# Kernel tuning notes

Hardware: AMD Instinct MI355X
Metric: run time of the kernel (lower is better)

## Reference

```python
import jax, jax.numpy as jnp
import numpy as np

B, L_PREM, T_HYP, D = 32, 256, 128, 256


def setup_inputs() -> dict:
    key = jax.random.key(0)
    ks = jax.random.split(key, 6)
    scale = 1.0 / np.sqrt(D)
    return {
        "x": jax.random.normal(ks[0], (B, L_PREM + T_HYP, D), dtype=jnp.float32),
        "w_y": jax.random.normal(ks[1], (D, D), dtype=jnp.float32) * scale,
        "w_h": jax.random.normal(ks[2], (D, D), dtype=jnp.float32) * scale,
        "w_r": jax.random.normal(ks[3], (D, D), dtype=jnp.float32) * scale,
        "w_alpha": jax.random.normal(ks[4], (D, 1), dtype=jnp.float32) * scale,
        "w_t": jax.random.normal(ks[5], (D, D), dtype=jnp.float32) * scale,
        "L": L_PREM,
    }


def reference(x, w_y, w_h, w_r, w_alpha, w_t, L):
    # x: (B, L + T, D)
    premise = x[:, :L, :]                 # Y: (B, L, D)
    hypothesis = jnp.swapaxes(x[:, L:, :], 0, 1)  # (T, B, D)

    # Y @ W_y does not depend on t: hoist out of the scan (same math).
    WY = jnp.einsum("bld,de->ble", premise, w_y)  # (B, L, D)

    def step(r_tm1, h_t):
        # r_tm1: (B, D), h_t: (B, D)
        s = h_t @ w_h + r_tm1 @ w_r                 # (B, D)
        Mt = jnp.tanh(WY + s[:, None, :])           # (B, L, D)
        scores = jnp.squeeze(Mt @ w_alpha, -1)      # (B, L)
        alpha = jax.nn.softmax(scores, axis=-1)     # (B, L)
        r_t = jnp.einsum("bl,bld->bd", alpha, premise) + r_tm1 @ w_t
        return r_t, r_t

    r0 = jnp.zeros_like(premise[:, 0, :])           # (B, D)
    _, rs = jax.lax.scan(step, r0, hypothesis)      # rs: (T, B, D)
    return jnp.swapaxes(rs, 0, 1)                   # (B, T, D)
```

## Files before the change

### kernel.cpp

```cpp
#include <hip/hip_runtime.h>
#include <hip/hip_fp16.h>

typedef unsigned long long u64;

#define C2X 2.8853900817779268f
#define LOG2E 1.4426950408889634f

#define WYS_OFF   0u
#define PR_OFF    4194304u
#define PREMH_OFF 8388608u
#define HWH_OFF   12582912u
#define WTH_OFF   16777216u
#define WTR_OFF   16908288u
#define ZP_OFF    17039360u
#define RCH_OFF   18087936u
#define MEMSET_SZ 1179648u

#define PRC_OFF    0u
#define WTRC_OFF   16384u
#define PREMC_OFF  32768u
#define WTC_OFF    49152u
#define WYC_OFF    65536u
#define HWHC_OFF   81920u
#define SCH_OFF    98304u
#define WACH_OFF   98432u
#define RED_OFF    98560u
#define ALB_OFF    98624u
#define RBB_OFF    100672u
#define PART_OFF   101696u
#define LDS_TOTAL  105920u

__global__ __launch_bounds__(256) void prep_all(const float* __restrict__ x,
                                                const float* __restrict__ wy,
                                                const float* __restrict__ wh,
                                                const float* __restrict__ wr,
                                                const float* __restrict__ wt,
                                                __half* __restrict__ wys,
                                                __half* __restrict__ prh,
                                                float* __restrict__ hwh,
                                                __half* __restrict__ wtrh,
                                                __half* __restrict__ premh,
                                                __half* __restrict__ wth) {
    const int blk = blockIdx.x;
    if (blk >= 1568) {
        int i = (blk - 1568) * 256 + threadIdx.x;
        float4 v; __half* dst; int e;
        if (i < 524288) {
            e = i * 4; int b = e >> 16;
            v = *(const float4*)(x + (size_t)e + (size_t)b * 32768);
            dst = premh + e;
        } else if (i < 540672) {
            e = (i - 524288) * 4;
            v = *(const float4*)(wt + e);
            dst = wth + e;
        } else return;
        __half h[4] = {__float2half(v.x),__float2half(v.y),__float2half(v.z),__float2half(v.w)};
        *(uint2*)dst = *(const uint2*)h;
        return;
    }
    __shared__ float At[8][256];
    const int d = threadIdx.x;
    int mode, row0;
    if (blk < 1024)      { mode = 0; row0 = blk * 8; }
    else if (blk < 1536) { mode = 1; row0 = (blk - 1024) * 8; }
    else                 { mode = 2; row0 = (blk - 1536) * 8; }
    for (int rr = 0; rr < 8; ++rr) {
        int r = row0 + rr;
        const float* src;
        if (mode == 0)      { int b = r >> 8, l = r & 255; src = x + (size_t)(b * 384 + l) * 256; }
        else if (mode == 1) { int tt = r >> 5, bb = r & 31; src = x + (size_t)(bb * 384 + 256 + tt) * 256; }
        else                { src = wt + (size_t)r * 256; }
        At[rr][d] = src[d];
    }
    __syncthreads();
    if (mode == 0) {
        float accy[8] = {0,0,0,0,0,0,0,0}, accr[8] = {0,0,0,0,0,0,0,0};
        for (int k = 0; k < 256; k += 2) {
            float y0 = wy[(size_t)k * 256 + d], y1 = wy[(size_t)(k + 1) * 256 + d];
            float r0 = wr[(size_t)k * 256 + d], r1 = wr[(size_t)(k + 1) * 256 + d];
#pragma unroll
            for (int rr = 0; rr < 8; ++rr) {
                float2 a = *(const float2*)&At[rr][k];
                accy[rr] = fmaf(a.x, y0, accy[rr]); accy[rr] = fmaf(a.y, y1, accy[rr]);
                accr[rr] = fmaf(a.x, r0, accr[rr]); accr[rr] = fmaf(a.y, r1, accr[rr]);
            }
        }
        for (int rr = 0; rr < 8; ++rr) {
            int r = row0 + rr;
            wys[(size_t)r * 256 + d] = __float2half(accy[rr] * C2X);
            prh[(size_t)r * 256 + d] = __float2half(accr[rr]);
        }
    } else {
        const float* w = (mode == 1) ? wh : wr;
        float acc[8] = {0,0,0,0,0,0,0,0};
        for (int k = 0; k < 256; k += 4) {
            float w0 = w[(size_t)k * 256 + d], w1 = w[(size_t)(k+1) * 256 + d];
            float w2 = w[(size_t)(k+2) * 256 + d], w3 = w[(size_t)(k+3) * 256 + d];
#pragma unroll
            for (int rr = 0; rr < 8; ++rr) {
                float4 a = *(const float4*)&At[rr][k];
                float t0 = fmaf(a.x, w0, acc[rr]);
                t0 = fmaf(a.y, w1, t0);
                t0 = fmaf(a.z, w2, t0);
                acc[rr] = fmaf(a.w, w3, t0);
            }
        }
        for (int rr = 0; rr < 8; ++rr) {
            int r = row0 + rr;
            if (mode == 1) hwh[(size_t)r * 256 + d] = acc[rr] * C2X;
            else           wtrh[(size_t)r * 256 + d] = __float2half(acc[rr]);
        }
    }
}

__device__ __forceinline__ u64 agent_load64(const u64* p) {
    return __hip_atomic_load(p, __ATOMIC_RELAXED, __HIP_MEMORY_SCOPE_AGENT);
}
__device__ __forceinline__ void agent_store64(u64* p, u64 v) {
    __hip_atomic_store(p, v, __ATOMIC_RELAXED, __HIP_MEMORY_SCOPE_AGENT);
}

__global__ __launch_bounds__(512, 1) void wbw_main(
    const __half* __restrict__ wys, const __half* __restrict__ prh,
    const __half* __restrict__ premh, const __half* __restrict__ wth,
    const __half* __restrict__ wtrh, const float* __restrict__ hwh,
    const float* __restrict__ walpha, float* __restrict__ out,
    u64* __restrict__ zp, u64* __restrict__ rch)
{
    extern __shared__ char lds[];
    const int tid = threadIdx.x;
    const int b = blockIdx.x >> 3, j = blockIdx.x & 7;

    float* hwhc  = (float*)(lds + HWHC_OFF);
    float* s_ch  = (float*)(lds + SCH_OFF);
    float* wa_ch = (float*)(lds + WACH_OFF);
    float* redb  = (float*)(lds + RED_OFF);
    float* alb   = (float*)(lds + ALB_OFF);
    float* rbb   = (float*)(lds + RBB_OFF);
    float* part  = (float*)(lds + PART_OFF);

    {
        const int prt = tid & 3;
        for (int it = 0; it < 2; ++it) {
            int row = it * 128 + (tid >> 2);
            size_t g = (size_t)row * 256 + j * 32 + prt * 8;
            unsigned lo = (unsigned)row * 64 + (unsigned)prt * 16;
            *(uint4*)(lds + PRC_OFF   + lo) = *(const uint4*)(prh   + (size_t)b * 65536 + g);
            *(uint4*)(lds + WTRC_OFF  + lo) = *(const uint4*)(wtrh  + g);
            *(uint4*)(lds + PREMC_OFF + lo) = *(const uint4*)(premh + (size_t)b * 65536 + g);
            *(uint4*)(lds + WTC_OFF   + lo) = *(const uint4*)(wth   + g);
            *(uint4*)(lds + WYC_OFF   + lo) = *(const uint4*)(wys   + (size_t)b * 65536 + g);
        }
    }
    for (int it = 0; it < 8; ++it) {
        int idx = it * 512 + tid;
        int tt = idx >> 5, dd = idx & 31;
        hwhc[idx] = hwh[((size_t)tt * 32 + b) * 256 + j * 32 + dd];
    }
    if (tid < 32)  wa_ch[tid] = walpha[j * 32 + tid] * (-2.0f * LOG2E);
    if (tid < 256) { alb[tid] = 0.f; alb[256 + tid] = 0.f; rbb[tid] = 0.f; }
    if (tid < 8)   redb[tid] = (tid == 0 || tid == 4) ? 1.f : 0.f;
    __syncthreads();

    for (int t = 0; t <= 128; ++t) {
        const int par = t & 1, q = par ^ 1;
        const float* e1 = alb + q * 256;

        {
            const int sel = tid >> 7;
            const int s8  = (tid >> 4) & 7;
            const int d0  = (tid & 15) * 2;
            const __half* mat = (const __half*)(lds + (unsigned)sel * 16384u);
            const float* vec = (sel & 1) ? rbb : e1;
            float ax = 0.f, ay = 0.f;
#pragma unroll
            for (int i = 0; i < 32; ++i) {
                int l = s8 + i * 8;
                float v = vec[l];
                float2 mf = __half22float2(*(const __half2*)&mat[l * 32 + d0]);
                ax = fmaf(v, mf.x, ax); ay = fmaf(v, mf.y, ay);
            }
            const int row = tid >> 4;
            part[row * 33 + d0] = ax; part[row * 33 + d0 + 1] = ay;
        }
        __syncthreads();

        if (tid < 64) {
            const int d = tid & 31;
            const float* rd = redb + q * 4;
            float rD = __builtin_amdgcn_rcpf(rd[0] + rd[1] + rd[2] + rd[3]);
            if (tid < 32) {
                if (t < 128) {
                    float sa = 0.f, sb = 0.f;
#pragma unroll
                    for (int s = 0; s < 8; ++s)  sa += part[s * 33 + d];
#pragma unroll
                    for (int s = 8; s < 16; ++s) sb += part[s * 33 + d];
                    s_ch[d] = fmaf(fmaf(sa, rD, sb), C2X, hwhc[t * 32 + d]);
                }
            } else {
                float ra = 0.f, rb2 = 0.f;
#pragma unroll
                for (int s = 16; s < 24; ++s) ra  += part[s * 33 + d];
#pragma unroll
                for (int s = 24; s < 32; ++s) rb2 += part[s * 33 + d];
                float rv = fmaf(ra, rD, rb2);
                if (t >= 1) out[((size_t)b * 128 + (t - 1)) * 256 + j * 32 + d] = rv;
                if (t < 128) {
                    u64 pk = ((u64)(unsigned)t << 32) | (u64)__float_as_uint(rv);
                    agent_store64(&rch[(size_t)(par * 32 + b) * 256 + j * 32 + d], pk);
                }
            }
        }
        __syncthreads();
        if (t == 128) break;

        {
            const int l = tid >> 1, dh = (tid & 1) << 4;
            union { uint4 u[2]; __half h[16]; } W;
            W.u[0] = *(const uint4*)(lds + WYC_OFF + (unsigned)l * 64 + (unsigned)dh * 2);
            W.u[1] = *(const uint4*)(lds + WYC_OFF + (unsigned)l * 64 + (unsigned)dh * 2 + 16);
            float acc = 0.f;
#pragma unroll
            for (int i = 0; i < 16; ++i) {
                float arg = __half2float(W.h[i]) + s_ch[dh + i];
                acc = fmaf(wa_ch[dh + i],
                           __builtin_amdgcn_rcpf(__builtin_amdgcn_exp2f(arg) + 1.f), acc);
            }
            acc += __shfl_xor(acc, 1, 64);
            if ((tid & 1) == 0) {
                u64 pk = ((u64)(unsigned)(t + 1) << 32) | (u64)__float_as_uint(acc);
                agent_store64(&zp[(size_t)((par * 32 + b) * 8 + j) * 256 + l], pk);
            }
        }

        if (tid < 256) {
            const u64* zb = zp + (size_t)(par * 32 + b) * 2048 + tid;
            u64 v0,v1,v2,v3,v4,v5,v6,v7; int tries = 0;
            for (;;) {
                v0 = agent_load64(zb);         v1 = agent_load64(zb + 256);
                v2 = agent_load64(zb + 512);   v3 = agent_load64(zb + 768);
                v4 = agent_load64(zb + 1024);  v5 = agent_load64(zb + 1280);
                v6 = agent_load64(zb + 1536);  v7 = agent_load64(zb + 1792);
                bool ok = ((unsigned)(v0 >> 32) > (unsigned)t) & ((unsigned)(v1 >> 32) > (unsigned)t)
                        & ((unsigned)(v2 >> 32) > (unsigned)t) & ((unsigned)(v3 >> 32) > (unsigned)t)
                        & ((unsigned)(v4 >> 32) > (unsigned)t) & ((unsigned)(v5 >> 32) > (unsigned)t)
                        & ((unsigned)(v6 >> 32) > (unsigned)t) & ((unsigned)(v7 >> 32) > (unsigned)t);
                if (__all(ok)) break;
                if (++tries > 2) __builtin_amdgcn_s_sleep(1);
            }
            float zs = __uint_as_float((unsigned)v0) + __uint_as_float((unsigned)v1)
                     + __uint_as_float((unsigned)v2) + __uint_as_float((unsigned)v3)
                     + __uint_as_float((unsigned)v4) + __uint_as_float((unsigned)v5)
                     + __uint_as_float((unsigned)v6) + __uint_as_float((unsigned)v7);
            float ee = __builtin_amdgcn_exp2f(zs);
            float sv = ee;
#pragma unroll
            for (int off = 32; off; off >>= 1) sv += __shfl_xor(sv, off, 64);
            if ((tid & 63) == 0) redb[par * 4 + (tid >> 6)] = sv;
            alb[par * 256 + tid] = ee;
        } else {
            const int t256 = tid - 256;
            const u64* rp = &rch[(size_t)(par * 32 + b) * 256 + t256];
            u64 rv;
            for (;;) {
                rv = agent_load64(rp);
                if (__all((unsigned)(rv >> 32) >= (unsigned)t)) break;
                __builtin_amdgcn_s_sleep(1);
            }
            rbb[t256] = __uint_as_float((unsigned)rv);
        }
        __syncthreads();
    }
}

extern "C" void kernel_launch(void* const* d_in, const int* in_sizes, int n_in,
                              void* d_out, int out_size, void* d_ws, size_t ws_size,
                              hipStream_t stream) {
    const float* x   = (const float*)d_in[0];
    const float* wy  = (const float*)d_in[1];
    const float* wh  = (const float*)d_in[2];
    const float* wr  = (const float*)d_in[3];
    const float* wal = (const float*)d_in[4];
    const float* wt  = (const float*)d_in[5];

    char* ws = (char*)d_ws;
    __half* wys    = (__half*)(ws + WYS_OFF);
    __half* prh    = (__half*)(ws + PR_OFF);
    __half* premh  = (__half*)(ws + PREMH_OFF);
    float*  hwh    = (float*)(ws + HWH_OFF);
    __half* wth    = (__half*)(ws + WTH_OFF);
    __half* wtrh   = (__half*)(ws + WTR_OFF);
    u64*    zp     = (u64*)(ws + ZP_OFF);
    u64*    rch    = (u64*)(ws + RCH_OFF);

    hipFuncSetAttribute((const void*)wbw_main,
                        hipFuncAttributeMaxDynamicSharedMemorySize, (int)LDS_TOTAL);

    prep_all<<<3680, 256, 0, stream>>>(x, wy, wh, wr, wt, wys, prh, hwh, wtrh, premh, wth);
    hipMemsetAsync(ws + ZP_OFF, 0, MEMSET_SZ, stream);

    wbw_main<<<256, 512, LDS_TOTAL, stream>>>(wys, prh, premh, wth, wtrh, hwh,
                                              wal, (float*)d_out, zp, rch);
}
```

Baseline: 474.7 us.

## Transpose and swizzle LDS matrices, fuse matvec reduction with shuffles, skip own-chunk r reload

Stores the four per-step matvec matrices in LDS transposed (d-major) with an XOR swizzle. This lets each thread read 8 contiguous l values per uint4 and reduce across lanes with shuffles, instead of writing partials to LDS and running a separate 64-thread reduction phase. That removes one __syncthreads and the partial buffer from the recurrent loop. It also swizzles the WY chunk to avoid bank conflicts, vectorizes the s_ch/wa_ch reads in the tanh stage, and double-buffers rbb so each block writes its own r chunk locally instead of polling global memory for it. The risks are a more complex setup, and the rbb double buffer must stay consistent across parity.

```diff
diff --git a/kernel.cpp b/kernel.cpp
--- a/kernel.cpp
+++ b/kernel.cpp
@@ -16,19 +16,18 @@
 #define RCH_OFF   18087936u
 #define MEMSET_SZ 1179648u
 
-#define PRC_OFF    0u
-#define WTRC_OFF   16384u
-#define PREMC_OFF  32768u
-#define WTC_OFF    49152u
+#define PRT_OFF    0u
+#define WTRT_OFF   16384u
+#define PREMT_OFF  32768u
+#define WTT_OFF    49152u
 #define WYC_OFF    65536u
 #define HWHC_OFF   81920u
 #define SCH_OFF    98304u
 #define WACH_OFF   98432u
 #define RED_OFF    98560u
 #define ALB_OFF    98624u
-#define RBB_OFF    100672u
-#define PART_OFF   101696u
-#define LDS_TOTAL  105920u
+#define RBB_OFF    100736u
+#define LDS_TOTAL  102848u
 
 __global__ __launch_bounds__(256) void prep_all(const float* __restrict__ x,
                                                 const float* __restrict__ wy,
@@ -137,19 +136,36 @@
     float* redb  = (float*)(lds + RED_OFF);
     float* alb   = (float*)(lds + ALB_OFF);
     float* rbb   = (float*)(lds + RBB_OFF);
-    float* part  = (float*)(lds + PART_OFF);
 
     {
-        const int prt = tid & 3;
+        const __half* srcs[4] = { prh + (size_t)b * 65536, wtrh,
+                                  premh + (size_t)b * 65536, wth };
+#pragma unroll
+        for (int m = 0; m < 4; ++m) {
+            const uint4* s = (const uint4*)srcs[m];
+            char* base = lds + (unsigned)m * 16384u;
+            for (int it = 0; it < 2; ++it) {
+                int idx = it * 512 + tid;
+                int l = idx >> 2, dq = idx & 3;
+                uint4 v = s[l * 32 + j * 4 + dq];
+                const __half* hp = (const __half*)&v;
+#pragma unroll
+                for (int k = 0; k < 8; ++k) {
+                    int d = dq * 8 + k;
+                    *(__half*)(base + (unsigned)d * 512u +
+                               (((unsigned)l * 2u) ^ ((unsigned)k << 4))) = hp[k];
+                }
+            }
+        }
+    }
+    {
+        const uint4* s = (const uint4*)(wys + (size_t)b * 65536);
         for (int it = 0; it < 2; ++it) {
-            int row = it * 128 + (tid >> 2);
-            size_t g = (size_t)row * 256 + j * 32 + prt * 8;
-            unsigned lo = (unsigned)row * 64 + (unsigned)prt * 16;
-            *(uint4*)(lds + PRC_OFF   + lo) = *(const uint4*)(prh   + (size_t)b * 65536 + g);
-            *(uint4*)(lds + WTRC_OFF  + lo) = *(const uint4*)(wtrh  + g);
-            *(uint4*)(lds + PREMC_OFF + lo) = *(const uint4*)(premh + (size_t)b * 65536 + g);
-            *(uint4*)(lds + WTC_OFF   + lo) = *(const uint4*)(wth   + g);
-            *(uint4*)(lds + WYC_OFF   + lo) = *(const uint4*)(wys   + (size_t)b * 65536 + g);
+            int idx = it * 512 + tid;
+            int l = idx >> 2, c = idx & 3;
+            uint4 v = s[l * 32 + j * 4 + c];
+            *(uint4*)(lds + WYC_OFF +
+                      (((unsigned)(l * 64 + c * 16)) ^ (((unsigned)l & 7u) << 4))) = v;
         }
     }
     for (int it = 0; it < 8; ++it) {
@@ -158,57 +174,63 @@
         hwhc[idx] = hwh[((size_t)tt * 32 + b) * 256 + j * 32 + dd];
     }
     if (tid < 32)  wa_ch[tid] = walpha[j * 32 + tid] * (-2.0f * LOG2E);
-    if (tid < 256) { alb[tid] = 0.f; alb[256 + tid] = 0.f; rbb[tid] = 0.f; }
+    if (tid < 256) { alb[tid] = 0.f; alb[264 + tid] = 0.f;
+                     rbb[tid] = 0.f; rbb[264 + tid] = 0.f; }
     if (tid < 8)   redb[tid] = (tid == 0 || tid == 4) ? 1.f : 0.f;
     __syncthreads();
 
     for (int t = 0; t <= 128; ++t) {
         const int par = t & 1, q = par ^ 1;
-        const float* e1 = alb + q * 256;
+        const float* e1 = alb + q * 264;
+        const float* rq = rbb + q * 264;
 
         {
-            const int sel = tid >> 7;
-            const int s8  = (tid >> 4) & 7;
-            const int d0  = (tid & 15) * 2;
-            const __half* mat = (const __half*)(lds + (unsigned)sel * 16384u);
-            const float* vec = (sel & 1) ? rbb : e1;
-            float ax = 0.f, ay = 0.f;
-#pragma unroll
-            for (int i = 0; i < 32; ++i) {
-                int l = s8 + i * 8;
-                float v = vec[l];
-                float2 mf = __half22float2(*(const __half2*)&mat[l * 32 + d0]);
-                ax = fmaf(v, mf.x, ax); ay = fmaf(v, mf.y, ay);
-            }
-            const int row = tid >> 4;
-            part[row * 33 + d0] = ax; part[row * 33 + d0 + 1] = ay;
-        }
-        __syncthreads();
-
-        if (tid < 64) {
-            const int d = tid & 31;
-            const float* rd = redb + q * 4;
-            float rD = __builtin_amdgcn_rcpf(rd[0] + rd[1] + rd[2] + rd[3]);
-            if (tid < 32) {
-                if (t < 128) {
-                    float sa = 0.f, sb = 0.f;
-#pragma unroll
-                    for (int s = 0; s < 8; ++s)  sa += part[s * 33 + d];
-#pragma unroll
-                    for (int s = 8; s < 16; ++s) sb += part[s * 33 + d];
-                    s_ch[d] = fmaf(fmaf(sa, rD, sb), C2X, hwhc[t * 32 + d]);
+            const int grp = tid >> 8;
+            const int k   = tid & 7;
+            const int lg  = (tid >> 3) & 7;
+            const int d   = ((tid >> 6) & 3) * 8 + k;
+            const int l0  = lg * 32;
+            if (grp == 0 ? (t < 128) : true) {
+                const char* mA = lds + (grp ? PREMT_OFF : PRT_OFF) + (unsigned)d * 512u;
+                const char* mB = lds + (grp ? WTT_OFF : WTRT_OFF) + (unsigned)d * 512u;
+                float ae = 0.f, ar = 0.f;
+#pragma unroll
+                for (int g = 0; g < 4; ++g) {
+                    unsigned off = ((unsigned)(l0 * 2 + g * 16)) ^ ((unsigned)k << 4);
+                    uint4 va = *(const uint4*)(mA + off);
+                    uint4 vb = *(const uint4*)(mB + off);
+                    const float4 e0 = *(const float4*)&e1[l0 + g * 8];
+                    const float4 e4 = *(const float4*)&e1[l0 + g * 8 + 4];
+                    const float4 r0 = *(const float4*)&rq[l0 + g * 8];
+                    const float4 r4 = *(const float4*)&rq[l0 + g * 8 + 4];
+                    const __half2* ha = (const __half2*)&va;
+                    const __half2* hb = (const __half2*)&vb;
+                    float2 f;
+                    f = __half22float2(ha[0]); ae = fmaf(e0.x, f.x, ae); ae = fmaf(e0.y, f.y, ae);
+                    f = __half22float2(ha[1]); ae = fmaf(e0.z, f.x, ae); ae = fmaf(e0.w, f.y, ae);
+                    f = __half22float2(ha[2]); ae = fmaf(e4.x, f.x, ae); ae = fmaf(e4.y, f.y, ae);
+                    f = __half22float2(ha[3]); ae = fmaf(e4.z, f.x, ae); ae = fmaf(e4.w, f.y, ae);
+                    f = __half22float2(hb[0]); ar = fmaf(r0.x, f.x, ar); ar = fmaf(r0.y, f.y, ar);
+                    f = __half22float2(hb[1]); ar = fmaf(r0.z, f.x, ar); ar = fmaf(r0.w, f.y, ar);
+                    f = __half22float2(hb[2]); ar = fmaf(r4.x, f.x, ar); ar = fmaf(r4.y, f.y, ar);
+                    f = __half22float2(hb[3]); ar = fmaf(r4.z, f.x, ar); ar = fmaf(r4.w, f.y, ar);
                 }
-            } else {
-                float ra = 0.f, rb2 = 0.f;
-#pragma unroll
-                for (int s = 16; s < 24; ++s) ra  += part[s * 33 + d];
-#pragma unroll
-                for (int s = 24; s < 32; ++s) rb2 += part[s * 33 + d];
-                float rv = fmaf(ra, rD, rb2);
-                if (t >= 1) out[((size_t)b * 128 + (t - 1)) * 256 + j * 32 + d] = rv;
-                if (t < 128) {
-                    u64 pk = ((u64)(unsigned)t << 32) | (u64)__float_as_uint(rv);
-                    agent_store64(&rch[(size_t)(par * 32 + b) * 256 + j * 32 + d], pk);
+                ae += __shfl_xor(ae, 8, 64);  ae += __shfl_xor(ae, 16, 64); ae += __shfl_xor(ae, 32, 64);
+                ar += __shfl_xor(ar, 8, 64);  ar += __shfl_xor(ar, 16, 64); ar += __shfl_xor(ar, 32, 64);
+                if (lg == 0) {
+                    const float* rd = redb + q * 4;
+                    float rD = __builtin_amdgcn_rcpf(rd[0] + rd[1] + rd[2] + rd[3]);
+                    float v = fmaf(ae, rD, ar);
+                    if (grp == 0) {
+                        s_ch[d] = fmaf(v, C2X, hwhc[t * 32 + d]);
+                    } else {
+                        if (t >= 1) out[((size_t)b * 128 + (t - 1)) * 256 + j * 32 + d] = v;
+                        rbb[par * 264 + j * 32 + d] = v;
+                        if (t < 128) {
+                            u64 pk = ((u64)(unsigned)t << 32) | (u64)__float_as_uint(v);
+                            agent_store64(&rch[(size_t)(par * 32 + b) * 256 + j * 32 + d], pk);
+                        }
+                    }
                 }
             }
         }
@@ -216,17 +238,41 @@
         if (t == 128) break;
 
         {
-            const int l = tid >> 1, dh = (tid & 1) << 4;
-            union { uint4 u[2]; __half h[16]; } W;
-            W.u[0] = *(const uint4*)(lds + WYC_OFF + (unsigned)l * 64 + (unsigned)dh * 2);
-            W.u[1] = *(const uint4*)(lds + WYC_OFF + (unsigned)l * 64 + (unsigned)dh * 2 + 16);
+            const int l = tid >> 1, c0 = (tid & 1) * 2, dh = (tid & 1) << 4;
+            const unsigned key = ((unsigned)l & 7u) << 4;
+            uint4 W0 = *(const uint4*)(lds + WYC_OFF + (((unsigned)(l * 64 + c0 * 16)) ^ key));
+            uint4 W1 = *(const uint4*)(lds + WYC_OFF + (((unsigned)(l * 64 + c0 * 16 + 16)) ^ key));
+            const float4 s0 = *(const float4*)&s_ch[dh];
+            const float4 s1 = *(const float4*)&s_ch[dh + 4];
+            const float4 s2 = *(const float4*)&s_ch[dh + 8];
+            const float4 s3 = *(const float4*)&s_ch[dh + 12];
+            const float4 w0 = *(const float4*)&wa_ch[dh];
+            const float4 w1 = *(const float4*)&wa_ch[dh + 4];
+            const float4 w2 = *(const float4*)&wa_ch[dh + 8];
+            const float4 w3 = *(const float4*)&wa_ch[dh + 12];
+            const __half2* h0 = (const __half2*)&W0;
+            const __half2* h1 = (const __half2*)&W1;
             float acc = 0.f;
-#pragma unroll
-            for (int i = 0; i < 16; ++i) {
-                float arg = __half2float(W.h[i]) + s_ch[dh + i];
-                acc = fmaf(wa_ch[dh + i],
-                           __builtin_amdgcn_rcpf(__builtin_amdgcn_exp2f(arg) + 1.f), acc);
-            }
+            float2 f;
+#define SIG(hh, sv, wv) { float arg = f.x + sv.x; acc = fmaf(wv.x, __builtin_amdgcn_rcpf(__builtin_amdgcn_exp2f(arg) + 1.f), acc); \
+                          arg = f.y + sv.y;      acc = fmaf(wv.y, __builtin_amdgcn_rcpf(__builtin_amdgcn_exp2f(arg) + 1.f), acc); }
+            f = __half22float2(h0[0]); { float arg = f.x + s0.x; acc = fmaf(w0.x, __builtin_amdgcn_rcpf(__builtin_amdgcn_exp2f(arg) + 1.f), acc);
+                                         arg = f.y + s0.y;       acc = fmaf(w0.y, __builtin_amdgcn_rcpf(__builtin_amdgcn_exp2f(arg) + 1.f), acc); }
+            f = __half22float2(h0[1]); { float arg = f.x + s0.z; acc = fmaf(w0.z, __builtin_amdgcn_rcpf(__builtin_amdgcn_exp2f(arg) + 1.f), acc);
+                                         arg = f.y + s0.w;       acc = fmaf(w0.w, __builtin_amdgcn_rcpf(__builtin_amdgcn_exp2f(arg) + 1.f), acc); }
+            f = __half22float2(h0[2]); { float arg = f.x + s1.x; acc = fmaf(w1.x, __builtin_amdgcn_rcpf(__builtin_amdgcn_exp2f(arg) + 1.f), acc);
+                                         arg = f.y + s1.y;       acc = fmaf(w1.y, __builtin_amdgcn_rcpf(__builtin_amdgcn_exp2f(arg) + 1.f), acc); }
+            f = __half22float2(h0[3]); { float arg = f.x + s1.z; acc = fmaf(w1.z, __builtin_amdgcn_rcpf(__builtin_amdgcn_exp2f(arg) + 1.f), acc);
+                                         arg = f.y + s1.w;       acc = fmaf(w1.w, __builtin_amdgcn_rcpf(__builtin_amdgcn_exp2f(arg) + 1.f), acc); }
+            f = __half22float2(h1[0]); { float arg = f.x + s2.x; acc = fmaf(w2.x, __builtin_amdgcn_rcpf(__builtin_amdgcn_exp2f(arg) + 1.f), acc);
+                                         arg = f.y + s2.y;       acc = fmaf(w2.y, __builtin_amdgcn_rcpf(__builtin_amdgcn_exp2f(arg) + 1.f), acc); }
+            f = __half22float2(h1[1]); { float arg = f.x + s2.z; acc = fmaf(w2.z, __builtin_amdgcn_rcpf(__builtin_amdgcn_exp2f(arg) + 1.f), acc);
+                                         arg = f.y + s2.w;       acc = fmaf(w2.w, __builtin_amdgcn_rcpf(__builtin_amdgcn_exp2f(arg) + 1.f), acc); }
+            f = __half22float2(h1[2]); { float arg = f.x + s3.x; acc = fmaf(w3.x, __builtin_amdgcn_rcpf(__builtin_amdgcn_exp2f(arg) + 1.f), acc);
+                                         arg = f.y + s3.y;       acc = fmaf(w3.y, __builtin_amdgcn_rcpf(__builtin_amdgcn_exp2f(arg) + 1.f), acc); }
+            f = __half22float2(h1[3]); { float arg = f.x + s3.z; acc = fmaf(w3.z, __builtin_amdgcn_rcpf(__builtin_amdgcn_exp2f(arg) + 1.f), acc);
+                                         arg = f.y + s3.w;       acc = fmaf(w3.w, __builtin_amdgcn_rcpf(__builtin_amdgcn_exp2f(arg) + 1.f), acc); }
+#undef SIG
             acc += __shfl_xor(acc, 1, 64);
             if ((tid & 1) == 0) {
                 u64 pk = ((u64)(unsigned)(t + 1) << 32) | (u64)__float_as_uint(acc);
@@ -258,17 +304,19 @@
 #pragma unroll
             for (int off = 32; off; off >>= 1) sv += __shfl_xor(sv, off, 64);
             if ((tid & 63) == 0) redb[par * 4 + (tid >> 6)] = sv;
-            alb[par * 256 + tid] = ee;
+            alb[par * 264 + tid] = ee;
         } else {
             const int t256 = tid - 256;
-            const u64* rp = &rch[(size_t)(par * 32 + b) * 256 + t256];
-            u64 rv;
-            for (;;) {
-                rv = agent_load64(rp);
-                if (__all((unsigned)(rv >> 32) >= (unsigned)t)) break;
-                __builtin_amdgcn_s_sleep(1);
-            }
-            rbb[t256] = __uint_as_float((unsigned)rv);
+            if ((t256 >> 5) != j) {
+                const u64* rp = &rch[(size_t)(par * 32 + b) * 256 + t256];
+                u64 rv;
+                for (;;) {
+                    rv = agent_load64(rp);
+                    if (__all((unsigned)(rv >> 32) >= (unsigned)t)) break;
+                    __builtin_amdgcn_s_sleep(1);
+                }
+                rbb[par * 264 + t256] = __uint_as_float((unsigned)rv);
+            }
         }
         __syncthreads();
     }
```

Result: faster. 458.7 us (-3.4%).
